# Performance work log

Hardware: AMD Instinct MI355X
Metric: run time of the kernel (lower is better)

## Reference

```python
import jax, jax.numpy as jnp
import numpy as np


def segment_softmax(scores, seg, num_segments):
    # numerically stable softmax over edges grouped by destination node
    m = jax.ops.segment_max(scores, seg, num_segments=num_segments)
    e = jnp.exp(scores - m[seg])
    d = jax.ops.segment_sum(e, seg, num_segments=num_segments)
    return e / d[seg]


def setup_inputs() -> dict:
    key = jax.random.key(0)
    ks = jax.random.split(key, 13)
    N, E, D = 50000, 400000, 128
    s = 0.02
    return {
        "x": jax.random.normal(ks[0], (N, D), dtype=jnp.float32),
        "t": jax.random.normal(ks[1], (N, D), dtype=jnp.float32),
        "edge_index": jax.random.randint(ks[2], (2, E), 0, N),
        "W_x": jax.random.normal(ks[3], (D, D), dtype=jnp.float32) * s,
        "W_t": jax.random.normal(ks[4], (D, D), dtype=jnp.float32) * s,
        "Q_alpha_w": jax.random.normal(ks[5], (D, D), dtype=jnp.float32) * s,
        "Q_alpha_b": jax.random.normal(ks[6], (D,), dtype=jnp.float32) * s,
        "K_alpha_w": jax.random.normal(ks[7], (D, D), dtype=jnp.float32) * s,
        "K_alpha_b": jax.random.normal(ks[8], (D,), dtype=jnp.float32) * s,
        "Q_beta_w": jax.random.normal(ks[9], (D, D), dtype=jnp.float32) * s,
        "Q_beta_b": jax.random.normal(ks[10], (D,), dtype=jnp.float32) * s,
        "K_beta_w": jax.random.normal(ks[11], (D, D), dtype=jnp.float32) * s,
        "K_beta_b": jax.random.normal(ks[12], (D,), dtype=jnp.float32) * s,
    }


def reference(x, t, edge_index, W_x, W_t, Q_alpha_w, Q_alpha_b,
              K_alpha_w, K_alpha_b, Q_beta_w, Q_beta_b, K_beta_w, K_beta_b):
    N, D = x.shape
    row, col = edge_index[0], edge_index[1]  # row = dest (i), col = src (j)
    inv_sqrt_d = 1.0 / (D ** 0.5)

    # Linear projections on nodes, then gather per edge (same math as
    # projecting the gathered edge features, since Linear is per-row).
    q_alpha = (t @ Q_alpha_w.T + Q_alpha_b)[row]   # [E, D]
    k_alpha = (t @ K_alpha_w.T + K_alpha_b)[col]   # [E, D]
    alpha_scores = jnp.sum(q_alpha * k_alpha, axis=-1) * inv_sqrt_d  # [E]
    alpha = segment_softmax(alpha_scores, row, N)  # [E]

    q_beta = (x @ Q_beta_w.T + Q_beta_b)[row]
    k_beta = (x @ K_beta_w.T + K_beta_b)[col]
    beta_scores = jnp.sum(q_beta * k_beta, axis=-1) * inv_sqrt_d
    beta = segment_softmax(beta_scores, row, N)

    msg_for_t = alpha[:, None] * (t @ W_t.T)[col]  # [E, D]
    msg_for_x = beta[:, None] * (x @ W_x.T)[col]   # [E, D]

    out_x = jax.ops.segment_sum(msg_for_x, row, num_segments=N)  # [N, D]
    out_t = jax.ops.segment_sum(msg_for_t, row, num_segments=N)  # [N, D]
    return (out_x, out_t)
```

## Files before the change

### kernel.cpp

```cpp
#include <hip/hip_runtime.h>

__device__ __forceinline__ unsigned short f2bf(float f) {
    unsigned int x = __float_as_uint(f);
    x += 0x7fffu + ((x >> 16) & 1u);
    return (unsigned short)(x >> 16);
}
__device__ __forceinline__ float2 bf2x(unsigned int u) {
    float2 r;
    r.x = __uint_as_float(u << 16);
    r.y = __uint_as_float(u & 0xffff0000u);
    return r;
}
template <int CTRL>
__device__ __forceinline__ float dppadd(float v) {
    int r = __builtin_amdgcn_mov_dpp(__float_as_uint(v), CTRL, 0xf, 0xf, true);
    return v + __uint_as_float(r);
}
__device__ __forceinline__ float red16(float v) {
    v = dppadd<0xB1>(v);
    v = dppadd<0x4E>(v);
    v = dppadd<0x141>(v);
    v = dppadd<0x140>(v);
    return v;
}
__device__ __forceinline__ float dot8(const uint4& A, const float* q) {
    float2 f; float p = 0.f;
    f = bf2x(A.x); p = fmaf(q[0], f.x, fmaf(q[1], f.y, p));
    f = bf2x(A.y); p = fmaf(q[2], f.x, fmaf(q[3], f.y, p));
    f = bf2x(A.z); p = fmaf(q[4], f.x, fmaf(q[5], f.y, p));
    f = bf2x(A.w); p = fmaf(q[6], f.x, fmaf(q[7], f.y, p));
    return p;
}
__device__ __forceinline__ void axpy8(const uint4& A, float w, float* acc) {
    float2 f;
    f = bf2x(A.x); acc[0] = fmaf(w, f.x, acc[0]); acc[1] = fmaf(w, f.y, acc[1]);
    f = bf2x(A.y); acc[2] = fmaf(w, f.x, acc[2]); acc[3] = fmaf(w, f.y, acc[3]);
    f = bf2x(A.z); acc[4] = fmaf(w, f.x, acc[4]); acc[5] = fmaf(w, f.y, acc[5]);
    f = bf2x(A.w); acc[6] = fmaf(w, f.x, acc[6]); acc[7] = fmaf(w, f.y, acc[7]);
}

typedef __attribute__((ext_vector_type(8))) short frag8;
typedef __attribute__((ext_vector_type(4))) float fragf4;

#define MAXDEG 64


__global__ __launch_bounds__(256) void prep_convert_hist(
    const float* __restrict__ Qa_w, const float* __restrict__ Ka_w,
    const float* __restrict__ Qa_b,
    const float* __restrict__ Qb_w, const float* __restrict__ Kb_w,
    const float* __restrict__ Qb_b,
    const float* __restrict__ W_t, const float* __restrict__ W_x,
    unsigned short* __restrict__ Wbf, float* __restrict__ ba, float* __restrict__ bb,
    const int* __restrict__ row, int* __restrict__ deg, int* __restrict__ rank, int E)
{
    const int b = blockIdx.x;
    const int tid = threadIdx.x;
    const float sc = 0.08838834764831845f;

    if (b < 32) {
        const int m = b >> 4;
        const int ro = b & 15;
        const float* Kw = m ? Kb_w : Ka_w;
        const float* Qw = m ? Qb_w : Qa_w;
        const int r = ro * 8 + (tid >> 5);
        const int c0 = (tid & 31) * 4;
        float a0 = 0.f, a1 = 0.f, a2 = 0.f, a3 = 0.f;
#pragma unroll 4
        for (int ch = 0; ch < 128; ch++) {
            const float kv = Kw[ch * 128 + r];
            const float4 q = *(const float4*)(Qw + ch * 128 + c0);
            a0 = fmaf(kv, q.x, a0); a1 = fmaf(kv, q.y, a1);
            a2 = fmaf(kv, q.z, a2); a3 = fmaf(kv, q.w, a3);
        }
        const int ct = r >> 4, li = r & 15;
        const int ks = c0 >> 5, quad = (c0 >> 3) & 3, j = c0 & 7;
        ushort4 u;
        u.x = f2bf(a0 * sc); u.y = f2bf(a1 * sc);
        u.z = f2bf(a2 * sc); u.w = f2bf(a3 * sc);
        *(ushort4*)(Wbf + (size_t)m * 16384 +
                    ((size_t)((ct * 4 + ks) * 64 + quad * 16 + li)) * 8 + j) = u;
    } else if (b < 34) {
        const int m = b - 32;
        if (tid < 128) {
            const float* Kw = m ? Kb_w : Ka_w;
            const float* bq = m ? Qb_b : Qa_b;
            float a = 0.f;
#pragma unroll 4
            for (int ch = 0; ch < 128; ch++) a = fmaf(bq[ch], Kw[ch * 128 + tid], a);
            (m ? bb : ba)[tid] = a * sc;
        }
    } else if (b < 66) {
        const int cm = (b - 34) >> 4;
        const int local = (b - 34) & 15;
        const int id = local * 256 + tid;
        const int e4 = id * 4;
        const float* s = cm ? W_x : W_t;
        float4 v = *(const float4*)(s + e4);
        int r = e4 >> 7, c = e4 & 127;
        int ct = r >> 4, li = r & 15;
        int ks = c >> 5, quad = (c >> 3) & 3, j = c & 7;
        ushort4 u;
        u.x = f2bf(v.x); u.y = f2bf(v.y); u.z = f2bf(v.z); u.w = f2bf(v.w);
        *(ushort4*)(Wbf + (size_t)(2 + cm) * 16384 +
                    ((size_t)((ct * 4 + ks) * 64 + quad * 16 + li)) * 8 + j) = u;
    } else {
        int e = (b - 66) * 256 + tid;
        if (e < E) rank[e] = atomicAdd(&deg[row[e]], 1);
    }
}

#define TLROW 72
__global__ __launch_bounds__(256, 4) void proj_scatter(
    const float* __restrict__ in_t, const float* __restrict__ in_x, int N,
    const unsigned short* __restrict__ Wbf,
    const float* __restrict__ ba, const float* __restrict__ bb,
    unsigned short* __restrict__ q2ab, unsigned short* __restrict__ txb,
    const int* __restrict__ erow, const int* __restrict__ ecol,
    const int* __restrict__ rank, int* __restrict__ csr_col,
    int E, int nScat, int nbx)
{
    __shared__ __align__(16) unsigned short tile[4][16 * TLROW];

    if ((int)blockIdx.x < nScat) {
        int e = blockIdx.x * 256 + threadIdx.x;
        if (e < E) {
            const int rk = min(rank[e], MAXDEG - 1);
            csr_col[(size_t)erow[e] * MAXDEG + rk] = ecol[e];
        }
        return;
    }
    const int pb = blockIdx.x - nScat;
    const int bx = pb % nbx;
    const int rest = pb / nbx;
    const int p = rest & 1;
    const int cth = rest >> 1;

    const int wave = threadIdx.x >> 6;
    const int lane = threadIdx.x & 63;
    const int li = lane & 15, quad = lane >> 4;
    const int r0 = (bx * 4 + wave) * 16;
    if (r0 >= N) return;
    const int r = r0 + li;
    const bool rv = r < N;

    frag8 bt[4];
    {
        const float* inp = p ? in_x : in_t;
        const float* st = inp + (size_t)r * 128 + quad * 8;
#pragma unroll
        for (int ks = 0; ks < 4; ks++) {
            float4 lo = make_float4(0.f, 0.f, 0.f, 0.f), hi = lo;
            if (rv) {
                lo = *(const float4*)(st + ks * 32);
                hi = *(const float4*)(st + ks * 32 + 4);
            }
            frag8 f;
            f[0] = (short)f2bf(lo.x); f[1] = (short)f2bf(lo.y);
            f[2] = (short)f2bf(lo.z); f[3] = (short)f2bf(lo.w);
            f[4] = (short)f2bf(hi.x); f[5] = (short)f2bf(hi.y);
            f[6] = (short)f2bf(hi.z); f[7] = (short)f2bf(hi.w);
            bt[ks] = f;
        }
    }

    if (cth == 0 && rv) {
#pragma unroll
        for (int ks = 0; ks < 4; ks++)
            *(frag8*)(txb + (size_t)r * 256 + p * 128 + ks * 32 + quad * 8) = bt[ks];
    }

    const unsigned short* wb = Wbf + (size_t)p * 16384 + (size_t)cth * 8192
                             + (size_t)lane * 8;
    frag8 af[16];
#pragma unroll
    for (int u = 0; u < 16; u++)
        af[u] = *(const frag8*)(wb + u * 512);

    fragf4 acc[4];
#pragma unroll
    for (int ct = 0; ct < 4; ct++) acc[ct] = (fragf4){0.f, 0.f, 0.f, 0.f};
#pragma unroll
    for (int ct = 0; ct < 4; ct++) {
#pragma unroll
        for (int ks = 0; ks < 4; ks++)
            acc[ct] = __builtin_amdgcn_mfma_f32_16x16x32_bf16(
                af[ct * 4 + ks], bt[ks], acc[ct], 0, 0, 0);
    }

    const float* bias = (p ? bb : ba) + cth * 64;
    unsigned short* lt = &tile[wave][0];
#pragma unroll
    for (int ct = 0; ct < 4; ct++) {
        const int c = ct * 16 + quad * 4;
        float4 bv = *(const float4*)(bias + c);
        ushort4 u;
        u.x = f2bf(acc[ct][0] + bv.x);
        u.y = f2bf(acc[ct][1] + bv.y);
        u.z = f2bf(acc[ct][2] + bv.z);
        u.w = f2bf(acc[ct][3] + bv.w);
        *(ushort4*)&lt[li * TLROW + c] = u;
    }
    const int coff = p * 128 + cth * 64;
#pragma unroll
    for (int it = 0; it < 2; it++) {
        const int rr = it * 8 + (lane >> 3);
        const int cg = lane & 7;
        if (r0 + rr < N) {
            uint4 v = *(const uint4*)&lt[rr * TLROW + cg * 8];
            *(uint4*)(q2ab + (size_t)(r0 + rr) * 256 + coff + cg * 8) = v;
        }
    }
}

__global__ __launch_bounds__(256) void edge_fused(
    const unsigned short* __restrict__ q2ab, const unsigned short* __restrict__ txb,
    const unsigned short* __restrict__ Wbf,
    const int* __restrict__ csr_col, const int* __restrict__ deg,
    float* __restrict__ out_x, float* __restrict__ out_t, int N)
{
    __shared__ __align__(16) unsigned short tile[16][264];
    const int tid = threadIdx.x;
    const int wv = tid >> 6, lane = tid & 63;
    const int g = lane >> 4, sub = lane & 15;
    const int nblk = blockIdx.x * 16;
    if (nblk >= N) return;
    const int n = nblk + wv * 4 + g;
    const bool nv = n < N;

    float qa_r[8], qb_r[8];
    if (nv) {
        uint4 a = *(const uint4*)(q2ab + (size_t)n * 256 + sub * 8);
        uint4 b = *(const uint4*)(q2ab + (size_t)n * 256 + 128 + sub * 8);
        float2 f;
        f = bf2x(a.x); qa_r[0] = f.x; qa_r[1] = f.y;
        f = bf2x(a.y); qa_r[2] = f.x; qa_r[3] = f.y;
        f = bf2x(a.z); qa_r[4] = f.x; qa_r[5] = f.y;
        f = bf2x(a.w); qa_r[6] = f.x; qa_r[7] = f.y;
        f = bf2x(b.x); qb_r[0] = f.x; qb_r[1] = f.y;
        f = bf2x(b.y); qb_r[2] = f.x; qb_r[3] = f.y;
        f = bf2x(b.z); qb_r[4] = f.x; qb_r[5] = f.y;
        f = bf2x(b.w); qb_r[6] = f.x; qb_r[7] = f.y;
    } else {
#pragma unroll
        for (int j = 0; j < 8; j++) { qa_r[j] = 0.f; qb_r[j] = 0.f; }
    }

    const int s = nv ? n * MAXDEG : 0;
    const int e = nv ? s + min(deg[n], MAXDEG) : 0;

    float aggt[8], aggx[8];
#pragma unroll
    for (int j = 0; j < 8; j++) { aggt[j] = 0.f; aggx[j] = 0.f; }
    float dda = 0.f, ddb = 0.f;

    if (e > s) {
        for (int i = s; i < e; i += 4) {
            const int rem = e - i;
            const int cA = csr_col[i];
            const int cB = csr_col[(rem > 1) ? i + 1 : i];
            const int cC = csr_col[(rem > 2) ? i + 2 : i];
            const int cD = csr_col[(rem > 3) ? i + 3 : i];
            const unsigned short* rA = txb + (size_t)cA * 256;
            const unsigned short* rB = txb + (size_t)cB * 256;
            const unsigned short* rC = txb + (size_t)cC * 256;
            const unsigned short* rD = txb + (size_t)cD * 256;
            const uint4 tA = *(const uint4*)(rA + sub * 8);
            const uint4 xA = *(const uint4*)(rA + 128 + sub * 8);
            const uint4 tB = *(const uint4*)(rB + sub * 8);
            const uint4 xB = *(const uint4*)(rB + 128 + sub * 8);
            const uint4 tC = *(const uint4*)(rC + sub * 8);
            const uint4 xC = *(const uint4*)(rC + 128 + sub * 8);
            const uint4 tD = *(const uint4*)(rD + sub * 8);
            const uint4 xD = *(const uint4*)(rD + 128 + sub * 8);

            float paA = dot8(tA, qa_r), pbA = dot8(xA, qb_r);
            float paB = dot8(tB, qa_r), pbB = dot8(xB, qb_r);
            float paC = dot8(tC, qa_r), pbC = dot8(xC, qb_r);
            float paD = dot8(tD, qa_r), pbD = dot8(xD, qb_r);

            paA = red16(paA); pbA = red16(pbA);
            paB = red16(paB); pbB = red16(pbB);
            paC = red16(paC); pbC = red16(pbC);
            paD = red16(paD); pbD = red16(pbD);

            const float eaA = __expf(fminf(paA, 60.f));
            const float ebA = __expf(fminf(pbA, 60.f));
            const float eaB = (rem > 1) ? __expf(fminf(paB, 60.f)) : 0.f;
            const float ebB = (rem > 1) ? __expf(fminf(pbB, 60.f)) : 0.f;
            const float eaC = (rem > 2) ? __expf(fminf(paC, 60.f)) : 0.f;
            const float ebC = (rem > 2) ? __expf(fminf(pbC, 60.f)) : 0.f;
            const float eaD = (rem > 3) ? __expf(fminf(paD, 60.f)) : 0.f;
            const float ebD = (rem > 3) ? __expf(fminf(pbD, 60.f)) : 0.f;
            dda += (eaA + eaB) + (eaC + eaD);
            ddb += (ebA + ebB) + (ebC + ebD);

            axpy8(tA, eaA, aggt); axpy8(xA, ebA, aggx);
            axpy8(tB, eaB, aggt); axpy8(xB, ebB, aggx);
            axpy8(tC, eaC, aggt); axpy8(xC, ebC, aggx);
            axpy8(tD, eaD, aggt); axpy8(xD, ebD, aggx);
        }
    }

    const float ra = (dda > 0.f) ? 1.f / dda : 0.f;
    const float rb = (ddb > 0.f) ? 1.f / ddb : 0.f;
    const int rowi = wv * 4 + g;
    frag8 ut, ux;
#pragma unroll
    for (int j = 0; j < 8; j++) {
        ut[j] = (short)f2bf(aggt[j] * ra);
        ux[j] = (short)f2bf(aggx[j] * rb);
    }
    *(frag8*)&tile[rowi][sub * 8] = ut;
    *(frag8*)&tile[rowi][128 + sub * 8] = ux;
    __syncthreads();

    const int m = wv >> 1, chunk = wv & 1;
    const int li = lane & 15, quad = lane >> 4;
    frag8 bt[4];
#pragma unroll
    for (int ks = 0; ks < 4; ks++)
        bt[ks] = *(const frag8*)&tile[li][m * 128 + ks * 32 + quad * 8];
    const unsigned short* wbp = Wbf + (size_t)(2 + m) * 16384 + (size_t)chunk * 8192
                              + (size_t)lane * 8;
    frag8 af[16];
#pragma unroll
    for (int u = 0; u < 16; u++)
        af[u] = *(const frag8*)(wbp + u * 512);
    fragf4 acc[4];
#pragma unroll
    for (int ct = 0; ct < 4; ct++) acc[ct] = (fragf4){0.f, 0.f, 0.f, 0.f};
#pragma unroll
    for (int ct = 0; ct < 4; ct++) {
#pragma unroll
        for (int ks = 0; ks < 4; ks++)
            acc[ct] = __builtin_amdgcn_mfma_f32_16x16x32_bf16(
                af[ct * 4 + ks], bt[ks], acc[ct], 0, 0, 0);
    }
    if (nblk + li < N) {
        float* outp = (m ? out_x : out_t) + (size_t)(nblk + li) * 128 + chunk * 64;
#pragma unroll
        for (int ct = 0; ct < 4; ct++)
            *(float4*)(outp + ct * 16 + quad * 4) =
                make_float4(acc[ct][0], acc[ct][1], acc[ct][2], acc[ct][3]);
    }
}

extern "C" void kernel_launch(void* const* d_in, const int* in_sizes, int n_in,
                              void* d_out, int out_size, void* d_ws, size_t ws_size,
                              hipStream_t stream) {
    const float* x    = (const float*)d_in[0];
    const float* t    = (const float*)d_in[1];
    const int*   ei   = (const int*)d_in[2];
    const float* W_x  = (const float*)d_in[3];
    const float* W_t  = (const float*)d_in[4];
    const float* Qa_w = (const float*)d_in[5];
    const float* Qa_b = (const float*)d_in[6];
    const float* Ka_w = (const float*)d_in[7];
    const float* Qb_w = (const float*)d_in[9];
    const float* Qb_b = (const float*)d_in[10];
    const float* Kb_w = (const float*)d_in[11];

    const int N = in_sizes[0] / 128;
    const int E = in_sizes[2] / 2;
    const int* row = ei;
    const int* col = ei + E;

    char* ws = (char*)d_ws;
    size_t off = 0;
    auto carve = [&](size_t bytes) -> void* {
        void* p = ws + off;
        off += (bytes + 255) & ~(size_t)255;
        return p;
    };
    unsigned short* q2ab = (unsigned short*)carve((size_t)N * 256 * 2);
    unsigned short* txb  = (unsigned short*)carve((size_t)N * 256 * 2);
    int* deg      = (int*)carve((size_t)N * 4);
    int* rank     = (int*)carve((size_t)E * 4);
    int* csr_col  = (int*)carve((size_t)N * MAXDEG * 4);
    unsigned short* Wbf = (unsigned short*)carve((size_t)4 * 16384 * 2);
    float* ba = (float*)carve(128 * 4);
    float* bb = (float*)carve(128 * 4);

    (void)hipMemsetAsync(deg, 0, (size_t)N * 4, stream);

    dim3 b256(256);
    const int nHist = (E + 255) / 256;
    prep_convert_hist<<<dim3(66 + nHist), b256, 0, stream>>>(
        Qa_w, Ka_w, Qa_b, Qb_w, Kb_w, Qb_b, W_t, W_x, Wbf, ba, bb, row, deg, rank, E);

    const int nbx = (N + 63) / 64;
    const int nScat = (E + 255) / 256;
    proj_scatter<<<dim3(nScat + nbx * 4), b256, 0, stream>>>(
        t, x, N, Wbf, ba, bb, q2ab, txb,
        row, col, rank, csr_col, E, nScat, nbx);

    float* out_x = (float*)d_out;
    float* out_t = out_x + (size_t)N * 128;
    edge_fused<<<dim3((N + 15) / 16), b256, 0, stream>>>(
        q2ab, txb, Wbf, csr_col, deg, out_x, out_t, N);
}
```

Baseline: 221.5 us.

## Remap edge aggregation to one wavefront per destination node

The edge_fused kernel now gives each destination node a whole 64-lane wavefront instead of a 16-lane group. Lanes 0-31 handle the t/alpha half and lanes 32-63 the x/beta half, four bf16 features per lane. Score reduction extends to 32 lanes with a ds_swizzle step, and blocks grow to 1024 threads covering 16 nodes. This aims to stop one high-degree node from stalling three other nodes in the same wave and to cut per-lane register use. In exchange, each lane loads narrower 8-byte vectors, and 12 of the 16 waves sit idle during the MFMA output projection.

```diff
diff --git a/kernel.cpp b/kernel.cpp
--- a/kernel.cpp
+++ b/kernel.cpp
@@ -16,27 +16,17 @@
     int r = __builtin_amdgcn_mov_dpp(__float_as_uint(v), CTRL, 0xf, 0xf, true);
     return v + __uint_as_float(r);
 }
-__device__ __forceinline__ float red16(float v) {
+template <int PAT>
+__device__ __forceinline__ float swzadd(float v) {
+    return v + __uint_as_float(__builtin_amdgcn_ds_swizzle(__float_as_uint(v), PAT));
+}
+__device__ __forceinline__ float red32(float v) {
     v = dppadd<0xB1>(v);
     v = dppadd<0x4E>(v);
     v = dppadd<0x141>(v);
     v = dppadd<0x140>(v);
+    v = swzadd<0x401F>(v);
     return v;
-}
-__device__ __forceinline__ float dot8(const uint4& A, const float* q) {
-    float2 f; float p = 0.f;
-    f = bf2x(A.x); p = fmaf(q[0], f.x, fmaf(q[1], f.y, p));
-    f = bf2x(A.y); p = fmaf(q[2], f.x, fmaf(q[3], f.y, p));
-    f = bf2x(A.z); p = fmaf(q[4], f.x, fmaf(q[5], f.y, p));
-    f = bf2x(A.w); p = fmaf(q[6], f.x, fmaf(q[7], f.y, p));
-    return p;
-}
-__device__ __forceinline__ void axpy8(const uint4& A, float w, float* acc) {
-    float2 f;
-    f = bf2x(A.x); acc[0] = fmaf(w, f.x, acc[0]); acc[1] = fmaf(w, f.y, acc[1]);
-    f = bf2x(A.y); acc[2] = fmaf(w, f.x, acc[2]); acc[3] = fmaf(w, f.y, acc[3]);
-    f = bf2x(A.z); acc[4] = fmaf(w, f.x, acc[4]); acc[5] = fmaf(w, f.y, acc[5]);
-    f = bf2x(A.w); acc[6] = fmaf(w, f.x, acc[6]); acc[7] = fmaf(w, f.y, acc[7]);
 }
 
 typedef __attribute__((ext_vector_type(8))) short frag8;
@@ -213,7 +203,7 @@
     }
 }
 
-__global__ __launch_bounds__(256) void edge_fused(
+__global__ __launch_bounds__(1024) void edge_fused(
     const unsigned short* __restrict__ q2ab, const unsigned short* __restrict__ txb,
     const unsigned short* __restrict__ Wbf,
     const int* __restrict__ csr_col, const int* __restrict__ deg,
@@ -222,127 +212,108 @@
     __shared__ __align__(16) unsigned short tile[16][264];
     const int tid = threadIdx.x;
     const int wv = tid >> 6, lane = tid & 63;
-    const int g = lane >> 4, sub = lane & 15;
     const int nblk = blockIdx.x * 16;
-    if (nblk >= N) return;
-    const int n = nblk + wv * 4 + g;
+    const int n = nblk + wv;
     const bool nv = n < N;
 
-    float qa_r[8], qb_r[8];
+    const int side = lane >> 5;
+    const int idx  = lane & 31;
+    const int off  = side * 128 + idx * 4;
+
+    float q0 = 0.f, q1 = 0.f, q2 = 0.f, q3 = 0.f;
     if (nv) {
-        uint4 a = *(const uint4*)(q2ab + (size_t)n * 256 + sub * 8);
-        uint4 b = *(const uint4*)(q2ab + (size_t)n * 256 + 128 + sub * 8);
+        const uint2 qv = *(const uint2*)(q2ab + (size_t)n * 256 + off);
+        float2 f = bf2x(qv.x); q0 = f.x; q1 = f.y;
+        f = bf2x(qv.y); q2 = f.x; q3 = f.y;
+    }
+
+    float a0 = 0.f, a1 = 0.f, a2 = 0.f, a3 = 0.f, dd = 0.f;
+    const int dn = nv ? min(deg[n], MAXDEG) : 0;
+    const int s = n * MAXDEG;
+
+    for (int i = 0; i < dn; i += 4) {
+        const int rem = dn - i;
+        const int cA = csr_col[s + i];
+        const int cB = csr_col[s + ((rem > 1) ? i + 1 : i)];
+        const int cC = csr_col[s + ((rem > 2) ? i + 2 : i)];
+        const int cD = csr_col[s + ((rem > 3) ? i + 3 : i)];
+        const uint2 rA = *(const uint2*)(txb + (size_t)cA * 256 + off);
+        const uint2 rB = *(const uint2*)(txb + (size_t)cB * 256 + off);
+        const uint2 rC = *(const uint2*)(txb + (size_t)cC * 256 + off);
+        const uint2 rD = *(const uint2*)(txb + (size_t)cD * 256 + off);
+
         float2 f;
-        f = bf2x(a.x); qa_r[0] = f.x; qa_r[1] = f.y;
-        f = bf2x(a.y); qa_r[2] = f.x; qa_r[3] = f.y;
-        f = bf2x(a.z); qa_r[4] = f.x; qa_r[5] = f.y;
-        f = bf2x(a.w); qa_r[6] = f.x; qa_r[7] = f.y;
-        f = bf2x(b.x); qb_r[0] = f.x; qb_r[1] = f.y;
-        f = bf2x(b.y); qb_r[2] = f.x; qb_r[3] = f.y;
-        f = bf2x(b.z); qb_r[4] = f.x; qb_r[5] = f.y;
-        f = bf2x(b.w); qb_r[6] = f.x; qb_r[7] = f.y;
-    } else {
-#pragma unroll
-        for (int j = 0; j < 8; j++) { qa_r[j] = 0.f; qb_r[j] = 0.f; }
-    }
-
-    const int s = nv ? n * MAXDEG : 0;
-    const int e = nv ? s + min(deg[n], MAXDEG) : 0;
-
-    float aggt[8], aggx[8];
-#pragma unroll
-    for (int j = 0; j < 8; j++) { aggt[j] = 0.f; aggx[j] = 0.f; }
-    float dda = 0.f, ddb = 0.f;
-
-    if (e > s) {
-        for (int i = s; i < e; i += 4) {
-            const int rem = e - i;
-            const int cA = csr_col[i];
-            const int cB = csr_col[(rem > 1) ? i + 1 : i];
-            const int cC = csr_col[(rem > 2) ? i + 2 : i];
-            const int cD = csr_col[(rem > 3) ? i + 3 : i];
-            const unsigned short* rA = txb + (size_t)cA * 256;
-            const unsigned short* rB = txb + (size_t)cB * 256;
-            const unsigned short* rC = txb + (size_t)cC * 256;
-            const unsigned short* rD = txb + (size_t)cD * 256;
-            const uint4 tA = *(const uint4*)(rA + sub * 8);
-            const uint4 xA = *(const uint4*)(rA + 128 + sub * 8);
-            const uint4 tB = *(const uint4*)(rB + sub * 8);
-            const uint4 xB = *(const uint4*)(rB + 128 + sub * 8);
-            const uint4 tC = *(const uint4*)(rC + sub * 8);
-            const uint4 xC = *(const uint4*)(rC + 128 + sub * 8);
-            const uint4 tD = *(const uint4*)(rD + sub * 8);
-            const uint4 xD = *(const uint4*)(rD + 128 + sub * 8);
-
-            float paA = dot8(tA, qa_r), pbA = dot8(xA, qb_r);
-            float paB = dot8(tB, qa_r), pbB = dot8(xB, qb_r);
-            float paC = dot8(tC, qa_r), pbC = dot8(xC, qb_r);
-            float paD = dot8(tD, qa_r), pbD = dot8(xD, qb_r);
-
-            paA = red16(paA); pbA = red16(pbA);
-            paB = red16(paB); pbB = red16(pbB);
-            paC = red16(paC); pbC = red16(pbC);
-            paD = red16(paD); pbD = red16(pbD);
-
-            const float eaA = __expf(fminf(paA, 60.f));
-            const float ebA = __expf(fminf(pbA, 60.f));
-            const float eaB = (rem > 1) ? __expf(fminf(paB, 60.f)) : 0.f;
-            const float ebB = (rem > 1) ? __expf(fminf(pbB, 60.f)) : 0.f;
-            const float eaC = (rem > 2) ? __expf(fminf(paC, 60.f)) : 0.f;
-            const float ebC = (rem > 2) ? __expf(fminf(pbC, 60.f)) : 0.f;
-            const float eaD = (rem > 3) ? __expf(fminf(paD, 60.f)) : 0.f;
-            const float ebD = (rem > 3) ? __expf(fminf(pbD, 60.f)) : 0.f;
-            dda += (eaA + eaB) + (eaC + eaD);
-            ddb += (ebA + ebB) + (ebC + ebD);
-
-            axpy8(tA, eaA, aggt); axpy8(xA, ebA, aggx);
-            axpy8(tB, eaB, aggt); axpy8(xB, ebB, aggx);
-            axpy8(tC, eaC, aggt); axpy8(xC, ebC, aggx);
-            axpy8(tD, eaD, aggt); axpy8(xD, ebD, aggx);
-        }
-    }
-
-    const float ra = (dda > 0.f) ? 1.f / dda : 0.f;
-    const float rb = (ddb > 0.f) ? 1.f / ddb : 0.f;
-    const int rowi = wv * 4 + g;
-    frag8 ut, ux;
-#pragma unroll
-    for (int j = 0; j < 8; j++) {
-        ut[j] = (short)f2bf(aggt[j] * ra);
-        ux[j] = (short)f2bf(aggx[j] * rb);
-    }
-    *(frag8*)&tile[rowi][sub * 8] = ut;
-    *(frag8*)&tile[rowi][128 + sub * 8] = ux;
+        float vA0, vA1, vA2, vA3, vB0, vB1, vB2, vB3;
+        float vC0, vC1, vC2, vC3, vD0, vD1, vD2, vD3;
+        f = bf2x(rA.x); vA0 = f.x; vA1 = f.y;
+        f = bf2x(rA.y); vA2 = f.x; vA3 = f.y;
+        f = bf2x(rB.x); vB0 = f.x; vB1 = f.y;
+        f = bf2x(rB.y); vB2 = f.x; vB3 = f.y;
+        f = bf2x(rC.x); vC0 = f.x; vC1 = f.y;
+        f = bf2x(rC.y); vC2 = f.x; vC3 = f.y;
+        f = bf2x(rD.x); vD0 = f.x; vD1 = f.y;
+        f = bf2x(rD.y); vD2 = f.x; vD3 = f.y;
+
+        float pA = fmaf(q0, vA0, fmaf(q1, vA1, fmaf(q2, vA2, q3 * vA3)));
+        float pB = fmaf(q0, vB0, fmaf(q1, vB1, fmaf(q2, vB2, q3 * vB3)));
+        float pC = fmaf(q0, vC0, fmaf(q1, vC1, fmaf(q2, vC2, q3 * vC3)));
+        float pD = fmaf(q0, vD0, fmaf(q1, vD1, fmaf(q2, vD2, q3 * vD3)));
+
+        pA = red32(pA); pB = red32(pB); pC = red32(pC); pD = red32(pD);
+
+        const float eA = __expf(fminf(pA, 60.f));
+        const float eB = (rem > 1) ? __expf(fminf(pB, 60.f)) : 0.f;
+        const float eC = (rem > 2) ? __expf(fminf(pC, 60.f)) : 0.f;
+        const float eD = (rem > 3) ? __expf(fminf(pD, 60.f)) : 0.f;
+        dd += (eA + eB) + (eC + eD);
+
+        a0 = fmaf(eA, vA0, a0); a1 = fmaf(eA, vA1, a1);
+        a2 = fmaf(eA, vA2, a2); a3 = fmaf(eA, vA3, a3);
+        a0 = fmaf(eB, vB0, a0); a1 = fmaf(eB, vB1, a1);
+        a2 = fmaf(eB, vB2, a2); a3 = fmaf(eB, vB3, a3);
+        a0 = fmaf(eC, vC0, a0); a1 = fmaf(eC, vC1, a1);
+        a2 = fmaf(eC, vC2, a2); a3 = fmaf(eC, vC3, a3);
+        a0 = fmaf(eD, vD0, a0); a1 = fmaf(eD, vD1, a1);
+        a2 = fmaf(eD, vD2, a2); a3 = fmaf(eD, vD3, a3);
+    }
+
+    const float rcp = (dd > 0.f) ? 1.f / dd : 0.f;
+    ushort4 u;
+    u.x = f2bf(a0 * rcp); u.y = f2bf(a1 * rcp);
+    u.z = f2bf(a2 * rcp); u.w = f2bf(a3 * rcp);
+    *(ushort4*)&tile[wv][off] = u;
     __syncthreads();
 
-    const int m = wv >> 1, chunk = wv & 1;
-    const int li = lane & 15, quad = lane >> 4;
-    frag8 bt[4];
-#pragma unroll
-    for (int ks = 0; ks < 4; ks++)
-        bt[ks] = *(const frag8*)&tile[li][m * 128 + ks * 32 + quad * 8];
-    const unsigned short* wbp = Wbf + (size_t)(2 + m) * 16384 + (size_t)chunk * 8192
-                              + (size_t)lane * 8;
-    frag8 af[16];
-#pragma unroll
-    for (int u = 0; u < 16; u++)
-        af[u] = *(const frag8*)(wbp + u * 512);
-    fragf4 acc[4];
-#pragma unroll
-    for (int ct = 0; ct < 4; ct++) acc[ct] = (fragf4){0.f, 0.f, 0.f, 0.f};
-#pragma unroll
-    for (int ct = 0; ct < 4; ct++) {
+    if (wv < 4) {
+        const int m = wv >> 1, chunk = wv & 1;
+        const int li = lane & 15, quad = lane >> 4;
+        frag8 bt[4];
 #pragma unroll
         for (int ks = 0; ks < 4; ks++)
-            acc[ct] = __builtin_amdgcn_mfma_f32_16x16x32_bf16(
-                af[ct * 4 + ks], bt[ks], acc[ct], 0, 0, 0);
-    }
-    if (nblk + li < N) {
-        float* outp = (m ? out_x : out_t) + (size_t)(nblk + li) * 128 + chunk * 64;
-#pragma unroll
-        for (int ct = 0; ct < 4; ct++)
-            *(float4*)(outp + ct * 16 + quad * 4) =
-                make_float4(acc[ct][0], acc[ct][1], acc[ct][2], acc[ct][3]);
+            bt[ks] = *(const frag8*)&tile[li][m * 128 + ks * 32 + quad * 8];
+        const unsigned short* wbp = Wbf + (size_t)(2 + m) * 16384
+                                  + (size_t)chunk * 8192 + (size_t)lane * 8;
+        frag8 af[16];
+#pragma unroll
+        for (int uu = 0; uu < 16; uu++)
+            af[uu] = *(const frag8*)(wbp + uu * 512);
+        fragf4 acc[4];
+#pragma unroll
+        for (int ct = 0; ct < 4; ct++) acc[ct] = (fragf4){0.f, 0.f, 0.f, 0.f};
+#pragma unroll
+        for (int ct = 0; ct < 4; ct++) {
+#pragma unroll
+            for (int ks = 0; ks < 4; ks++)
+                acc[ct] = __builtin_amdgcn_mfma_f32_16x16x32_bf16(
+                    af[ct * 4 + ks], bt[ks], acc[ct], 0, 0, 0);
+        }
+        if (nblk + li < N) {
+            float* outp = (m ? out_x : out_t) + (size_t)(nblk + li) * 128 + chunk * 64;
+#pragma unroll
+            for (int ct = 0; ct < 4; ct++)
+                *(float4*)(outp + ct * 16 + quad * 4) =
+                    make_float4(acc[ct][0], acc[ct][1], acc[ct][2], acc[ct][3]);
+        }
     }
 }
 
@@ -397,6 +368,6 @@
 
     float* out_x = (float*)d_out;
     float* out_t = out_x + (size_t)N * 128;
-    edge_fused<<<dim3((N + 15) / 16), b256, 0, stream>>>(
+    edge_fused<<<dim3((N + 15) / 16), dim3(1024), 0, stream>>>(
         q2ab, txb, Wbf, csr_col, deg, out_x, out_t, N);
 }
```

Result: slower. 226.3 us (+2.2%).
